# Kernel optimization log

Hardware: AMD Instinct MI355X
Metric: run time of the kernel (lower is better)

The kernel has to match this reference:

```python
import jax, jax.numpy as jnp
import numpy as np

L = 6      # num_coupling_layers
H = 256    # hidden_dims
B = 131072 # batch
D = 2      # sample_dims (fixed by masks)


def setup_inputs() -> dict:
    key = jax.random.key(0)
    ks = jax.random.split(key, 21)
    x = jax.random.uniform(ks[0], (B, D), jnp.float32, 1e-3, 1.0 - 1e-3)
    def w(k, shape):
        return jax.random.normal(k, shape, jnp.float32) * 0.05
    inp = {"x": x}
    shapes = {"W1": (L, D, H), "B1": (L, H), "W2": (L, H, H), "B2": (L, H),
              "W3": (L, H, H), "B3": (L, H), "W4": (L, H, H), "B4": (L, H),
              "W5": (L, H, D), "B5": (L, D)}
    i = 1
    for pref in ("s", "t"):
        for name, shp in shapes.items():
            inp[pref + name] = w(ks[i], shp)
            i += 1
    return inp


def _net(h, i, W1, B1, W2, B2, W3, B3, W4, B4, W5, B5, final_tanh):
    a = jax.nn.relu(h @ W1[i] + B1[i])
    a = jax.nn.relu(a @ W2[i] + B2[i])
    a = jax.nn.relu(a @ W3[i] + B3[i])
    a = jax.nn.relu(a @ W4[i] + B4[i])
    o = a @ W5[i] + B5[i]
    return jnp.tanh(o) if final_tanh else o


def reference(x, sW1, sB1, sW2, sB2, sW3, sB3, sW4, sB4, sW5, sB5,
              tW1, tB1, tW2, tB2, tW3, tB3, tW4, tB4, tW5, tB5):
    # masks alternate [0,1],[1,0]
    masks = jnp.asarray([[0.0, 1.0], [1.0, 0.0]] * (L // 2), jnp.float32)
    # logit transform
    x = -jnp.log(1.0 / x - 1.0)
    log_det_inv = jnp.zeros(x.shape[0], x.dtype)
    # training=True default -> direction = -1, gate = -1, reversed layer order
    for i in range(L - 1, -1, -1):
        m = masks[i]
        rm = 1.0 - m
        x_masked = x * m
        s = _net(x_masked, i, sW1, sB1, sW2, sB2, sW3, sB3, sW4, sB4, sW5, sB5, True) * rm
        t = _net(x_masked, i, tW1, tB1, tW2, tB2, tW3, tB3, tW4, tB4, tW5, tB5, False) * rm
        # rm*(x*exp(-s) - t*exp(-s)) + x_masked
        x = rm * ((x - t) * jnp.exp(-s)) + x_masked
        log_det_inv = log_det_inv - jnp.sum(s, axis=1)
    x = jax.nn.sigmoid(x)
    return x, log_det_inv
```

## Files before the change

### kernel.cpp

```cpp
#include <hip/hip_runtime.h>
#include <hip/hip_bf16.h>

#define LNUM 6
#define BATCH 131072

typedef __bf16 bf16x8 __attribute__((ext_vector_type(8)));
typedef float f32x16 __attribute__((ext_vector_type(16)));
typedef float f32x4  __attribute__((ext_vector_type(4)));

#define WFRAG_BYTES 131072ul
#define W1B1_OFF 4718592ul
#define BIAS_OFF 4743168ul
#define W5_OFF   4780032ul
#define NPT   2048
#define ZMIN  (-28.f)
#define ZH    (56.f / 2047.f)
#define ZINVH (2047.f / 56.f)
#define TABS_OFF 4793088ul
#define TABT_OFF 4842240ul
#define WS_NEEDED 4891392ul

struct PtrPack { const float* p[21]; };

__global__ void prep_all(PtrPack P, unsigned char* __restrict__ ws) {
    if (blockIdx.x < 1152) {
        int t = blockIdx.x * 256 + threadIdx.x;
        int blk = t >> 13;
        int e8  = t & 8191;
        int nh  = e8 >> 12;
        int kk  = (e8 >> 8) & 15;
        int nti = (e8 >> 6) & 3;
        int l   = e8 & 63;
        int nt = nh * 4 + nti;
        int n  = nt * 32 + (l & 31);
        int k0 = kk * 16 + (l >> 5) * 8;
        int net = blk / 18, rem = blk % 18;
        int i = rem / 3, g = rem % 3;
        const float* src = P.p[3 + g * 2 + net * 10] + i * 65536;
        bf16x8 v;
#pragma unroll
        for (int jj = 0; jj < 8; ++jj) v[jj] = (__bf16)src[(k0 + jj) * 256 + n];
        *(bf16x8*)(ws + (unsigned long)blk * WFRAG_BYTES + (unsigned)e8 * 16) = v;
        return;
    }
    int t = (blockIdx.x - 1152) * 256 + threadIdx.x;
    if (t < 6144) {
        int idx = t >> 9, e = t & 511;
        int net = idx / 6, i = idx % 6;
        int j = (i & 1) ? 0 : 1;
        float v;
        if (e < 256) v = P.p[1 + net * 10][i * 512 + j * 256 + e];
        else         v = P.p[2 + net * 10][i * 256 + (e - 256)];
        ((float*)(ws + W1B1_OFF))[t] = v;
    } else if (t < 6144 + 9216) {
        int u = t - 6144;
        int idx = u >> 8, e = u & 255;
        int net = idx / 18, rem = idx % 18, i = rem / 3, g = rem % 3;
        ((float*)(ws + BIAS_OFF))[u] = P.p[4 + g * 2 + net * 10][i * 256 + e];
    } else if (t < 6144 + 9216 + 12 * 272) {
        int u = t - 6144 - 9216;
        int idx = u / 272, e = u % 272;
        int net = idx / 6, i = idx % 6;
        int ud = (i & 1) ? 1 : 0;
        float v = 0.f;
        if (e < 256)      v = P.p[9 + net * 10][i * 512 + e * 2 + ud];
        else if (e == 256) v = P.p[10 + net * 10][i * 2 + ud];
        ((float*)(ws + W5_OFF))[idx * 272 + e] = v;
    }
}

#define L_A   0
#define L_ZG  65536
#define L_RED 67072
#define L_TOT 69632

__device__ __forceinline__ unsigned pk2(float a, float b) {
    unsigned short ua = __builtin_bit_cast(unsigned short, (__bf16)a);
    unsigned short ub = __builtin_bit_cast(unsigned short, (__bf16)b);
    return (unsigned)ua | ((unsigned)ub << 16);
}

__global__ __launch_bounds__(256, 2) void tab_eval(
        const unsigned char* __restrict__ ws, float* __restrict__ tabS,
        float* __restrict__ tabT) {
    __shared__ __align__(16) unsigned char lds[L_TOT];
    const int tid = threadIdx.x;
    const int wv = tid >> 6, lane = tid & 63;
    const int li = lane & 31, hi = lane >> 5;
    const int nn = blockIdx.x >> 4;
    const int tile = blockIdx.x & 15;
    float* zG  = (float*)(lds + L_ZG);
    float* red = (float*)(lds + L_RED);
    const float* w1b1_g = (const float*)(ws + W1B1_OFF);
    const float* bias_g = (const float*)(ws + BIAS_OFF);
    const float* w5_g   = (const float*)(ws + W5_OFF);

    const unsigned char* aaBase = lds + L_A + (unsigned)lane * 16;
    unsigned char* const stBase = lds + L_A + (unsigned)(li * 16 + hi * 8);

    if (tid < 128) zG[tid] = ZMIN + (float)(tile * 128 + tid) * ZH;
    __syncthreads();

    auto storeA = [&](const f32x16* a) {
#pragma unroll
        for (int rt = 0; rt < 4; ++rt)
#pragma unroll
            for (int j2 = 0; j2 < 2; ++j2)
#pragma unroll
                for (int q = 0; q < 4; ++q) {
                    const f32x16& A = a[rt * 2 + j2];
                    unsigned lo = pk2(fmaxf(A[4 * q + 0], 0.f), fmaxf(A[4 * q + 1], 0.f));
                    unsigned h2 = pk2(fmaxf(A[4 * q + 2], 0.f), fmaxf(A[4 * q + 3], 0.f));
                    const unsigned off = (unsigned)((wv * 4 + j2 * 2 + (q >> 1)) * 4096
                                                    + rt * 1024 + (q & 1) * 512);
                    *(uint2*)(stBase + off) = make_uint2(lo, h2);
                }
    };

    {
        const float* w1 = w1b1_g + nn * 512;
        bf16x8 wf[2], af[4];
        const bf16x8 zr = {};
        if (hi == 0) {
#pragma unroll
            for (int f = 0; f < 2; ++f) {
                const int n = (wv * 2 + f) * 32 + li;
                const float W = w1[n], B = w1[256 + n];
                const __bf16 Wh = (__bf16)W;
                const __bf16 Wl = (__bf16)(W - (float)Wh);
                const __bf16 Bh = (__bf16)B;
                const __bf16 Bl = (__bf16)(B - (float)Bh);
                bf16x8 t = zr;
                t[0] = Wh; t[1] = Wl; t[2] = Wh; t[3] = Bh; t[4] = Bl;
                wf[f] = t;
            }
#pragma unroll
            for (int rt = 0; rt < 4; ++rt) {
                const float z = zG[rt * 32 + li];
                const __bf16 zh = (__bf16)z;
                const __bf16 zl = (__bf16)(z - (float)zh);
                bf16x8 t = zr;
                t[0] = zh; t[1] = zh; t[2] = zl;
                t[3] = (__bf16)1.f; t[4] = (__bf16)1.f;
                af[rt] = t;
            }
        } else {
            wf[0] = zr; wf[1] = zr;
            af[0] = zr; af[1] = zr; af[2] = zr; af[3] = zr;
        }
        f32x16 acc1[8];
#pragma unroll
        for (int u = 0; u < 8; ++u)
#pragma unroll
            for (int e = 0; e < 16; ++e) acc1[u][e] = 0.f;
#pragma unroll
        for (int rt = 0; rt < 4; ++rt) {
            acc1[rt * 2 + 0] = __builtin_amdgcn_mfma_f32_32x32x16_bf16(wf[0], af[rt], acc1[rt * 2 + 0], 0, 0, 0);
            acc1[rt * 2 + 1] = __builtin_amdgcn_mfma_f32_32x32x16_bf16(wf[1], af[rt], acc1[rt * 2 + 1], 0, 0, 0);
        }
        storeA(acc1);
    }
    __syncthreads();

#pragma unroll 1
    for (int g = 0; g < 3; ++g) {
        const int blk = nn * 3 + g;
        const unsigned char* wbase = ws + (unsigned long)blk * WFRAG_BYTES
                + (unsigned)(wv >> 1) * 65536 + (unsigned)(wv & 1) * 2048
                + (unsigned)lane * 16;
        const float* biasl = bias_g + blk * 256 + wv * 64;
        const float* w5 = w5_g + nn * 272;

        f32x16 acc[8];
#pragma unroll
        for (int j2 = 0; j2 < 2; ++j2)
#pragma unroll
            for (int q = 0; q < 4; ++q) {
                f32x4 bb = *(const f32x4*)(biasl + j2 * 32 + q * 8 + hi * 4);
#pragma unroll
                for (int rt = 0; rt < 4; ++rt) {
                    acc[rt * 2 + j2][4 * q + 0] = bb[0];
                    acc[rt * 2 + j2][4 * q + 1] = bb[1];
                    acc[rt * 2 + j2][4 * q + 2] = bb[2];
                    acc[rt * 2 + j2][4 * q + 3] = bb[3];
                }
            }
        bf16x8 wq[3][2];
#pragma unroll
        for (int p = 0; p < 3; ++p) {
            wq[p][0] = *(const bf16x8*)(wbase + p * 4096);
            wq[p][1] = *(const bf16x8*)(wbase + p * 4096 + 1024);
        }
        bf16x8 aa[2][4];
#pragma unroll
        for (int rt = 0; rt < 4; ++rt)
            aa[0][rt] = *(const bf16x8*)(aaBase + rt * 1024);
#pragma unroll
        for (int k = 0; k < 16; ++k) {
            const int cur = k & 1, nxt = cur ^ 1;
            if (k < 15) {
#pragma unroll
                for (int rt = 0; rt < 4; ++rt)
                    aa[nxt][rt] = *(const bf16x8*)(aaBase + (k + 1) * 4096 + rt * 1024);
            }
            __builtin_amdgcn_s_setprio(1);
#pragma unroll
            for (int rt = 0; rt < 4; ++rt) {
                acc[rt * 2 + 0] = __builtin_amdgcn_mfma_f32_32x32x16_bf16(wq[k % 3][0], aa[cur][rt], acc[rt * 2 + 0], 0, 0, 0);
                acc[rt * 2 + 1] = __builtin_amdgcn_mfma_f32_32x32x16_bf16(wq[k % 3][1], aa[cur][rt], acc[rt * 2 + 1], 0, 0, 0);
            }
            __builtin_amdgcn_s_setprio(0);
            if (k < 13) {
                wq[k % 3][0] = *(const bf16x8*)(wbase + (k + 3) * 4096);
                wq[k % 3][1] = *(const bf16x8*)(wbase + (k + 3) * 4096 + 1024);
            }
        }
        __syncthreads();
        if (g < 2) {
            storeA(acc);
            __syncthreads();
        } else {
            float part[4] = {0.f, 0.f, 0.f, 0.f};
#pragma unroll
            for (int j2 = 0; j2 < 2; ++j2)
#pragma unroll
                for (int q = 0; q < 4; ++q) {
                    f32x4 ww = *(const f32x4*)(w5 + wv * 64 + j2 * 32 + q * 8 + hi * 4);
#pragma unroll
                    for (int rt = 0; rt < 4; ++rt)
#pragma unroll
                        for (int c = 0; c < 4; ++c)
                            part[rt] += fmaxf(acc[rt * 2 + j2][4 * q + c], 0.f) * ww[c];
                }
#pragma unroll
            for (int rt = 0; rt < 4; ++rt) part[rt] += __shfl_xor(part[rt], 32);
            if (hi == 0) {
#pragma unroll
                for (int rt = 0; rt < 4; ++rt) red[wv * 128 + rt * 32 + li] = part[rt];
            }
            __syncthreads();
            if (tid < 128) {
                const float o = red[tid] + red[128 + tid] + red[256 + tid] + red[384 + tid]
                                + w5[256];
                const int pt = (nn % 6) * NPT + tile * 128 + tid;
                if (nn < 6) tabS[pt] = tanhf(o);
                else        tabT[pt] = o;
            }
        }
    }
}

__global__ __launch_bounds__(256) void apply_flow(
        const float* __restrict__ x, const float* __restrict__ tabS,
        const float* __restrict__ tabT, float* __restrict__ out) {
    const int r = blockIdx.x * 256 + threadIdx.x;
    const float2 xv = ((const float2*)x)[r];
    float zA = __logf(xv.x) - __logf(1.f - xv.x);
    float zB = __logf(xv.y) - __logf(1.f - xv.y);
    float ldt = 0.f;
#pragma unroll
    for (int ii = 0; ii < LNUM; ++ii) {
        const int i = 5 - ii;
        const float zin = (i & 1) ? zA : zB;
        float u = (zin - ZMIN) * ZINVH;
        u = fminf(fmaxf(u, 0.f), (float)(NPT - 1) - 1e-3f);
        const int i0 = (int)u;
        const float fr = u - (float)i0;
        const float* ts = tabS + i * NPT + i0;
        const float* tt = tabT + i * NPT + i0;
        const float S = ts[0] + (ts[1] - ts[0]) * fr;
        const float T = tt[0] + (tt[1] - tt[0]) * fr;
        const float e = __expf(-S);
        if (i & 1) zB = (zB - T) * e;
        else       zA = (zA - T) * e;
        ldt -= S;
    }
    ((float2*)out)[r] = make_float2(1.f / (1.f + __expf(-zA)),
                                    1.f / (1.f + __expf(-zB)));
    out[2 * BATCH + r] = ldt;
}

extern "C" void kernel_launch(void* const* d_in, const int* in_sizes, int n_in,
                              void* d_out, int out_size, void* d_ws, size_t ws_size,
                              hipStream_t stream) {
    if (ws_size < WS_NEEDED) return;
    PtrPack P;
    for (int k = 0; k < 21; ++k) P.p[k] = (const float*)d_in[k];
    unsigned char* ws = (unsigned char*)d_ws;
    float* tabS = (float*)(ws + TABS_OFF);
    float* tabT = (float*)(ws + TABT_OFF);
    prep_all<<<dim3(1225), dim3(256), 0, stream>>>(P, ws);
    tab_eval<<<dim3(192), dim3(256), 0, stream>>>(ws, tabS, tabT);
    apply_flow<<<dim3(BATCH / 256), dim3(256), 0, stream>>>(
            (const float*)d_in[0], tabS, tabT, (float*)d_out);
}
```

Measured before the change: 30.26 us.

## Double tab_eval waves per block, coarsen prep and apply_flow threads

tab_eval moves from 256 to 512 threads per block. Each of the 8 waves now owns 32 output columns instead of 64, which halves accumulators and weight registers per wave and reduces across 8 partial sums instead of 4. prep_all now has each thread handle 4 (weight) or 8 (small-param) elements, cutting the grid from 1225 to 298 blocks. apply_flow handles two rows per thread with float4 loads and stores. The aim is more latency hiding in the table-eval stage and less launch and per-thread overhead elsewhere, at the cost of less parallelism in apply_flow and prep.

```diff
diff --git a/kernel.cpp b/kernel.cpp
--- a/kernel.cpp
+++ b/kernel.cpp
@@ -23,56 +23,62 @@
 struct PtrPack { const float* p[21]; };
 
 __global__ void prep_all(PtrPack P, unsigned char* __restrict__ ws) {
-    if (blockIdx.x < 1152) {
-        int t = blockIdx.x * 256 + threadIdx.x;
-        int blk = t >> 13;
-        int e8  = t & 8191;
-        int nh  = e8 >> 12;
-        int kk  = (e8 >> 8) & 15;
-        int nti = (e8 >> 6) & 3;
-        int l   = e8 & 63;
-        int nt = nh * 4 + nti;
-        int n  = nt * 32 + (l & 31);
-        int k0 = kk * 16 + (l >> 5) * 8;
-        int net = blk / 18, rem = blk % 18;
-        int i = rem / 3, g = rem % 3;
-        const float* src = P.p[3 + g * 2 + net * 10] + i * 65536;
-        bf16x8 v;
-#pragma unroll
-        for (int jj = 0; jj < 8; ++jj) v[jj] = (__bf16)src[(k0 + jj) * 256 + n];
-        *(bf16x8*)(ws + (unsigned long)blk * WFRAG_BYTES + (unsigned)e8 * 16) = v;
+    if (blockIdx.x < 288) {
+#pragma unroll
+        for (int r = 0; r < 4; ++r) {
+            int t = blockIdx.x * 1024 + r * 256 + threadIdx.x;
+            int blk = t >> 13;
+            int e8  = t & 8191;
+            int nh  = e8 >> 12;
+            int kk  = (e8 >> 8) & 15;
+            int nti = (e8 >> 6) & 3;
+            int l   = e8 & 63;
+            int nt = nh * 4 + nti;
+            int n  = nt * 32 + (l & 31);
+            int k0 = kk * 16 + (l >> 5) * 8;
+            int net = blk / 18, rem = blk % 18;
+            int i = rem / 3, g = rem % 3;
+            const float* src = P.p[3 + g * 2 + net * 10] + i * 65536;
+            bf16x8 v;
+#pragma unroll
+            for (int jj = 0; jj < 8; ++jj) v[jj] = (__bf16)src[(k0 + jj) * 256 + n];
+            *(bf16x8*)(ws + (unsigned long)blk * WFRAG_BYTES + (unsigned)e8 * 16) = v;
+        }
         return;
     }
-    int t = (blockIdx.x - 1152) * 256 + threadIdx.x;
-    if (t < 6144) {
-        int idx = t >> 9, e = t & 511;
-        int net = idx / 6, i = idx % 6;
-        int j = (i & 1) ? 0 : 1;
-        float v;
-        if (e < 256) v = P.p[1 + net * 10][i * 512 + j * 256 + e];
-        else         v = P.p[2 + net * 10][i * 256 + (e - 256)];
-        ((float*)(ws + W1B1_OFF))[t] = v;
-    } else if (t < 6144 + 9216) {
-        int u = t - 6144;
-        int idx = u >> 8, e = u & 255;
-        int net = idx / 18, rem = idx % 18, i = rem / 3, g = rem % 3;
-        ((float*)(ws + BIAS_OFF))[u] = P.p[4 + g * 2 + net * 10][i * 256 + e];
-    } else if (t < 6144 + 9216 + 12 * 272) {
-        int u = t - 6144 - 9216;
-        int idx = u / 272, e = u % 272;
-        int net = idx / 6, i = idx % 6;
-        int ud = (i & 1) ? 1 : 0;
-        float v = 0.f;
-        if (e < 256)      v = P.p[9 + net * 10][i * 512 + e * 2 + ud];
-        else if (e == 256) v = P.p[10 + net * 10][i * 2 + ud];
-        ((float*)(ws + W5_OFF))[idx * 272 + e] = v;
+#pragma unroll
+    for (int r = 0; r < 8; ++r) {
+        int t = (blockIdx.x - 288) * 2048 + r * 256 + threadIdx.x;
+        if (t < 6144) {
+            int idx = t >> 9, e = t & 511;
+            int net = idx / 6, i = idx % 6;
+            int j = (i & 1) ? 0 : 1;
+            float v;
+            if (e < 256) v = P.p[1 + net * 10][i * 512 + j * 256 + e];
+            else         v = P.p[2 + net * 10][i * 256 + (e - 256)];
+            ((float*)(ws + W1B1_OFF))[t] = v;
+        } else if (t < 6144 + 9216) {
+            int u = t - 6144;
+            int idx = u >> 8, e = u & 255;
+            int net = idx / 18, rem = idx % 18, i = rem / 3, g = rem % 3;
+            ((float*)(ws + BIAS_OFF))[u] = P.p[4 + g * 2 + net * 10][i * 256 + e];
+        } else if (t < 6144 + 9216 + 12 * 272) {
+            int u = t - 6144 - 9216;
+            int idx = u / 272, e = u % 272;
+            int net = idx / 6, i = idx % 6;
+            int ud = (i & 1) ? 1 : 0;
+            float v = 0.f;
+            if (e < 256)      v = P.p[9 + net * 10][i * 512 + e * 2 + ud];
+            else if (e == 256) v = P.p[10 + net * 10][i * 2 + ud];
+            ((float*)(ws + W5_OFF))[idx * 272 + e] = v;
+        }
     }
 }
 
 #define L_A   0
 #define L_ZG  65536
-#define L_RED 67072
-#define L_TOT 69632
+#define L_RED 66048
+#define L_TOT 70144
 
 __device__ __forceinline__ unsigned pk2(float a, float b) {
     unsigned short ua = __builtin_bit_cast(unsigned short, (__bf16)a);
@@ -80,7 +86,7 @@
     return (unsigned)ua | ((unsigned)ub << 16);
 }
 
-__global__ __launch_bounds__(256, 2) void tab_eval(
+__global__ __launch_bounds__(512, 1) void tab_eval(
         const unsigned char* __restrict__ ws, float* __restrict__ tabS,
         float* __restrict__ tabT) {
     __shared__ __align__(16) unsigned char lds[L_TOT];
@@ -105,59 +111,52 @@
 #pragma unroll
         for (int rt = 0; rt < 4; ++rt)
 #pragma unroll
-            for (int j2 = 0; j2 < 2; ++j2)
-#pragma unroll
-                for (int q = 0; q < 4; ++q) {
-                    const f32x16& A = a[rt * 2 + j2];
-                    unsigned lo = pk2(fmaxf(A[4 * q + 0], 0.f), fmaxf(A[4 * q + 1], 0.f));
-                    unsigned h2 = pk2(fmaxf(A[4 * q + 2], 0.f), fmaxf(A[4 * q + 3], 0.f));
-                    const unsigned off = (unsigned)((wv * 4 + j2 * 2 + (q >> 1)) * 4096
-                                                    + rt * 1024 + (q & 1) * 512);
-                    *(uint2*)(stBase + off) = make_uint2(lo, h2);
-                }
+            for (int q = 0; q < 4; ++q) {
+                const f32x16& A = a[rt];
+                unsigned lo = pk2(fmaxf(A[4 * q + 0], 0.f), fmaxf(A[4 * q + 1], 0.f));
+                unsigned h2 = pk2(fmaxf(A[4 * q + 2], 0.f), fmaxf(A[4 * q + 3], 0.f));
+                const unsigned off = (unsigned)((wv * 2 + (q >> 1)) * 4096
+                                                + rt * 1024 + (q & 1) * 512);
+                *(uint2*)(stBase + off) = make_uint2(lo, h2);
+            }
     };
 
     {
         const float* w1 = w1b1_g + nn * 512;
-        bf16x8 wf[2], af[4];
+        bf16x8 wf, af[4];
         const bf16x8 zr = {};
         if (hi == 0) {
-#pragma unroll
-            for (int f = 0; f < 2; ++f) {
-                const int n = (wv * 2 + f) * 32 + li;
-                const float W = w1[n], B = w1[256 + n];
-                const __bf16 Wh = (__bf16)W;
-                const __bf16 Wl = (__bf16)(W - (float)Wh);
-                const __bf16 Bh = (__bf16)B;
-                const __bf16 Bl = (__bf16)(B - (float)Bh);
-                bf16x8 t = zr;
-                t[0] = Wh; t[1] = Wl; t[2] = Wh; t[3] = Bh; t[4] = Bl;
-                wf[f] = t;
-            }
+            const int n = wv * 32 + li;
+            const float W = w1[n], B = w1[256 + n];
+            const __bf16 Wh = (__bf16)W;
+            const __bf16 Wl = (__bf16)(W - (float)Wh);
+            const __bf16 Bh = (__bf16)B;
+            const __bf16 Bl = (__bf16)(B - (float)Bh);
+            bf16x8 t = zr;
+            t[0] = Wh; t[1] = Wl; t[2] = Wh; t[3] = Bh; t[4] = Bl;
+            wf = t;
 #pragma unroll
             for (int rt = 0; rt < 4; ++rt) {
                 const float z = zG[rt * 32 + li];
                 const __bf16 zh = (__bf16)z;
                 const __bf16 zl = (__bf16)(z - (float)zh);
-                bf16x8 t = zr;
-                t[0] = zh; t[1] = zh; t[2] = zl;
-                t[3] = (__bf16)1.f; t[4] = (__bf16)1.f;
-                af[rt] = t;
+                bf16x8 t2 = zr;
+                t2[0] = zh; t2[1] = zh; t2[2] = zl;
+                t2[3] = (__bf16)1.f; t2[4] = (__bf16)1.f;
+                af[rt] = t2;
             }
         } else {
-            wf[0] = zr; wf[1] = zr;
+            wf = zr;
             af[0] = zr; af[1] = zr; af[2] = zr; af[3] = zr;
         }
-        f32x16 acc1[8];
-#pragma unroll
-        for (int u = 0; u < 8; ++u)
+        f32x16 acc1[4];
+#pragma unroll
+        for (int u = 0; u < 4; ++u)
 #pragma unroll
             for (int e = 0; e < 16; ++e) acc1[u][e] = 0.f;
 #pragma unroll
-        for (int rt = 0; rt < 4; ++rt) {
-            acc1[rt * 2 + 0] = __builtin_amdgcn_mfma_f32_32x32x16_bf16(wf[0], af[rt], acc1[rt * 2 + 0], 0, 0, 0);
-            acc1[rt * 2 + 1] = __builtin_amdgcn_mfma_f32_32x32x16_bf16(wf[1], af[rt], acc1[rt * 2 + 1], 0, 0, 0);
-        }
+        for (int rt = 0; rt < 4; ++rt)
+            acc1[rt] = __builtin_amdgcn_mfma_f32_32x32x16_bf16(wf, af[rt], acc1[rt], 0, 0, 0);
         storeA(acc1);
     }
     __syncthreads();
@@ -166,31 +165,27 @@
     for (int g = 0; g < 3; ++g) {
         const int blk = nn * 3 + g;
         const unsigned char* wbase = ws + (unsigned long)blk * WFRAG_BYTES
-                + (unsigned)(wv >> 1) * 65536 + (unsigned)(wv & 1) * 2048
+                + (unsigned)(wv >> 2) * 65536 + (unsigned)(wv & 3) * 1024
                 + (unsigned)lane * 16;
-        const float* biasl = bias_g + blk * 256 + wv * 64;
+        const float* biasl = bias_g + blk * 256 + wv * 32;
         const float* w5 = w5_g + nn * 272;
 
-        f32x16 acc[8];
-#pragma unroll
-        for (int j2 = 0; j2 < 2; ++j2)
-#pragma unroll
-            for (int q = 0; q < 4; ++q) {
-                f32x4 bb = *(const f32x4*)(biasl + j2 * 32 + q * 8 + hi * 4);
-#pragma unroll
-                for (int rt = 0; rt < 4; ++rt) {
-                    acc[rt * 2 + j2][4 * q + 0] = bb[0];
-                    acc[rt * 2 + j2][4 * q + 1] = bb[1];
-                    acc[rt * 2 + j2][4 * q + 2] = bb[2];
-                    acc[rt * 2 + j2][4 * q + 3] = bb[3];
-                }
-            }
-        bf16x8 wq[3][2];
-#pragma unroll
-        for (int p = 0; p < 3; ++p) {
-            wq[p][0] = *(const bf16x8*)(wbase + p * 4096);
-            wq[p][1] = *(const bf16x8*)(wbase + p * 4096 + 1024);
-        }
+        f32x16 acc[4];
+#pragma unroll
+        for (int q = 0; q < 4; ++q) {
+            f32x4 bb = *(const f32x4*)(biasl + q * 8 + hi * 4);
+#pragma unroll
+            for (int rt = 0; rt < 4; ++rt) {
+                acc[rt][4 * q + 0] = bb[0];
+                acc[rt][4 * q + 1] = bb[1];
+                acc[rt][4 * q + 2] = bb[2];
+                acc[rt][4 * q + 3] = bb[3];
+            }
+        }
+        bf16x8 wq[3];
+#pragma unroll
+        for (int p = 0; p < 3; ++p)
+            wq[p] = *(const bf16x8*)(wbase + p * 4096);
         bf16x8 aa[2][4];
 #pragma unroll
         for (int rt = 0; rt < 4; ++rt)
@@ -205,15 +200,11 @@
             }
             __builtin_amdgcn_s_setprio(1);
 #pragma unroll
-            for (int rt = 0; rt < 4; ++rt) {
-                acc[rt * 2 + 0] = __builtin_amdgcn_mfma_f32_32x32x16_bf16(wq[k % 3][0], aa[cur][rt], acc[rt * 2 + 0], 0, 0, 0);
-                acc[rt * 2 + 1] = __builtin_amdgcn_mfma_f32_32x32x16_bf16(wq[k % 3][1], aa[cur][rt], acc[rt * 2 + 1], 0, 0, 0);
-            }
+            for (int rt = 0; rt < 4; ++rt)
+                acc[rt] = __builtin_amdgcn_mfma_f32_32x32x16_bf16(wq[k % 3], aa[cur][rt], acc[rt], 0, 0, 0);
             __builtin_amdgcn_s_setprio(0);
-            if (k < 13) {
-                wq[k % 3][0] = *(const bf16x8*)(wbase + (k + 3) * 4096);
-                wq[k % 3][1] = *(const bf16x8*)(wbase + (k + 3) * 4096 + 1024);
-            }
+            if (k < 13)
+                wq[k % 3] = *(const bf16x8*)(wbase + (k + 3) * 4096);
         }
         __syncthreads();
         if (g < 2) {
@@ -222,16 +213,14 @@
         } else {
             float part[4] = {0.f, 0.f, 0.f, 0.f};
 #pragma unroll
-            for (int j2 = 0; j2 < 2; ++j2)
-#pragma unroll
-                for (int q = 0; q < 4; ++q) {
-                    f32x4 ww = *(const f32x4*)(w5 + wv * 64 + j2 * 32 + q * 8 + hi * 4);
-#pragma unroll
-                    for (int rt = 0; rt < 4; ++rt)
-#pragma unroll
-                        for (int c = 0; c < 4; ++c)
-                            part[rt] += fmaxf(acc[rt * 2 + j2][4 * q + c], 0.f) * ww[c];
-                }
+            for (int q = 0; q < 4; ++q) {
+                f32x4 ww = *(const f32x4*)(w5 + wv * 32 + q * 8 + hi * 4);
+#pragma unroll
+                for (int rt = 0; rt < 4; ++rt)
+#pragma unroll
+                    for (int c = 0; c < 4; ++c)
+                        part[rt] += fmaxf(acc[rt][4 * q + c], 0.f) * ww[c];
+            }
 #pragma unroll
             for (int rt = 0; rt < 4; ++rt) part[rt] += __shfl_xor(part[rt], 32);
             if (hi == 0) {
@@ -240,8 +229,9 @@
             }
             __syncthreads();
             if (tid < 128) {
-                const float o = red[tid] + red[128 + tid] + red[256 + tid] + red[384 + tid]
-                                + w5[256];
+                float o = w5[256];
+#pragma unroll
+                for (int w8 = 0; w8 < 8; ++w8) o += red[w8 * 128 + tid];
                 const int pt = (nn % 6) * NPT + tile * 128 + tid;
                 if (nn < 6) tabS[pt] = tanhf(o);
                 else        tabT[pt] = o;
@@ -254,30 +244,40 @@
         const float* __restrict__ x, const float* __restrict__ tabS,
         const float* __restrict__ tabT, float* __restrict__ out) {
     const int r = blockIdx.x * 256 + threadIdx.x;
-    const float2 xv = ((const float2*)x)[r];
-    float zA = __logf(xv.x) - __logf(1.f - xv.x);
-    float zB = __logf(xv.y) - __logf(1.f - xv.y);
-    float ldt = 0.f;
+    const float4 xv = ((const float4*)x)[r];
+    float zA0 = __logf(xv.x) - __logf(1.f - xv.x);
+    float zB0 = __logf(xv.y) - __logf(1.f - xv.y);
+    float zA1 = __logf(xv.z) - __logf(1.f - xv.z);
+    float zB1 = __logf(xv.w) - __logf(1.f - xv.w);
+    float ldt0 = 0.f, ldt1 = 0.f;
 #pragma unroll
     for (int ii = 0; ii < LNUM; ++ii) {
         const int i = 5 - ii;
-        const float zin = (i & 1) ? zA : zB;
-        float u = (zin - ZMIN) * ZINVH;
-        u = fminf(fmaxf(u, 0.f), (float)(NPT - 1) - 1e-3f);
-        const int i0 = (int)u;
-        const float fr = u - (float)i0;
-        const float* ts = tabS + i * NPT + i0;
-        const float* tt = tabT + i * NPT + i0;
-        const float S = ts[0] + (ts[1] - ts[0]) * fr;
-        const float T = tt[0] + (tt[1] - tt[0]) * fr;
-        const float e = __expf(-S);
-        if (i & 1) zB = (zB - T) * e;
-        else       zA = (zA - T) * e;
-        ldt -= S;
-    }
-    ((float2*)out)[r] = make_float2(1.f / (1.f + __expf(-zA)),
-                                    1.f / (1.f + __expf(-zB)));
-    out[2 * BATCH + r] = ldt;
+        const float* ts = tabS + i * NPT;
+        const float* tt = tabT + i * NPT;
+#pragma unroll
+        for (int rr = 0; rr < 2; ++rr) {
+            float& zA = rr ? zA1 : zA0;
+            float& zB = rr ? zB1 : zB0;
+            float& ldt = rr ? ldt1 : ldt0;
+            const float zin = (i & 1) ? zA : zB;
+            float u = (zin - ZMIN) * ZINVH;
+            u = fminf(fmaxf(u, 0.f), (float)(NPT - 1) - 1e-3f);
+            const int i0 = (int)u;
+            const float fr = u - (float)i0;
+            const float S = ts[i0] + (ts[i0 + 1] - ts[i0]) * fr;
+            const float T = tt[i0] + (tt[i0 + 1] - tt[i0]) * fr;
+            const float e = __expf(-S);
+            if (i & 1) zB = (zB - T) * e;
+            else       zA = (zA - T) * e;
+            ldt -= S;
+        }
+    }
+    ((float4*)out)[r] = make_float4(1.f / (1.f + __expf(-zA0)),
+                                    1.f / (1.f + __expf(-zB0)),
+                                    1.f / (1.f + __expf(-zA1)),
+                                    1.f / (1.f + __expf(-zB1)));
+    ((float2*)(out + 2 * BATCH))[r] = make_float2(ldt0, ldt1);
 }
 
 extern "C" void kernel_launch(void* const* d_in, const int* in_sizes, int n_in,
@@ -289,8 +289,8 @@
     unsigned char* ws = (unsigned char*)d_ws;
     float* tabS = (float*)(ws + TABS_OFF);
     float* tabT = (float*)(ws + TABT_OFF);
-    prep_all<<<dim3(1225), dim3(256), 0, stream>>>(P, ws);
-    tab_eval<<<dim3(192), dim3(256), 0, stream>>>(ws, tabS, tabT);
-    apply_flow<<<dim3(BATCH / 256), dim3(256), 0, stream>>>(
+    prep_all<<<dim3(298), dim3(256), 0, stream>>>(P, ws);
+    tab_eval<<<dim3(192), dim3(512), 0, stream>>>(ws, tabS, tabT);
+    apply_flow<<<dim3(BATCH / 512), dim3(256), 0, stream>>>(
             (const float*)d_in[0], tabS, tabT, (float*)d_out);
 }
```

After: 33.02 us. 9.1% more time.
